# Kernel optimization log

Measured on AMD Instinct MI355X. Metric: run time of the kernel, lower is better.

Reference implementation:

```python
import jax, jax.numpy as jnp
import numpy as np

FS, R, ULAW = 160, 2, 256  # frame_size, n_samples_per_step, 2**ulaw


def _conv1d(x, w, b):
    # x: [B,C,L], w: [O,I,3], VALID conv (PyTorch Conv1d, no padding)
    y = jax.lax.conv_general_dilated(x, w, (1,), 'VALID',
                                     dimension_numbers=('NCH', 'OIH', 'NCH'))
    return y + b[None, :, None]


def _gru(x, Wih, Whh, bih, bhh):
    # PyTorch GRU (batch_first), gate order r,z,n. x: [B,T,In] -> [B,T,H]
    B = x.shape[0]
    H = Whh.shape[1]
    xW = jnp.einsum('bti,gi->btg', x, Wih) + bih  # precompute input gates [B,T,3H]
    def step(h, xw):
        gh = h @ Whh.T + bhh
        r = jax.nn.sigmoid(xw[:, :H] + gh[:, :H])
        z = jax.nn.sigmoid(xw[:, H:2 * H] + gh[:, H:2 * H])
        n = jnp.tanh(xw[:, 2 * H:] + r * gh[:, 2 * H:])
        h = (1.0 - z) * n + z * h
        return h, h
    h0 = jnp.zeros((B, H), x.dtype)
    _, ys = jax.lax.scan(step, h0, jnp.swapaxes(xW, 0, 1))
    return jnp.swapaxes(ys, 0, 1)


def _mdense(x, w1, w2, b1, b2, f1, f2):
    return jnp.tanh(x @ w1.T + b1) * f1 + jnp.tanh(x @ w2.T + b2) * f2


def setup_inputs() -> dict:
    key = jax.random.key(0)
    ks = jax.random.split(key, 40)
    B, NF, NBF = 64, 15, 20
    T = (NF - 4) * FS  # 1760: two VALID k=3 convs -> 11 frames
    EP, ES, DF, H1, H2 = 64, 128, 128, 384, 16
    IN_A = 3 * ES * R + DF   # 896
    IN_B = H1 + DF           # 512
    p = lambda k, shape, s=0.1: (s * jax.random.normal(k, shape)).astype(jnp.float32)
    d = {
        'in_data': jax.random.randint(ks[0], (B, T, 3), 0, ULAW),
        'features': jax.random.normal(ks[1], (B, NF, NBF), jnp.float32),
        'periods': jax.random.randint(ks[2], (B, NF, 1), 0, 256),
        'targets': jax.random.randint(ks[3], (B, T), 0, ULAW),
        'embed_pitch': p(ks[4], (256, EP)),
        'embed_sig': p(ks[5], (ULAW, ES)),
        'conv1_w': p(ks[6], (DF, EP + NBF, 3)), 'conv1_b': p(ks[7], (DF,)),
        'conv2_w': p(ks[8], (DF, DF, 3)), 'conv2_b': p(ks[9], (DF,)),
        'fd1_w': p(ks[10], (DF, DF)), 'fd1_b': p(ks[11], (DF,)),
        'fd2_w': p(ks[12], (DF, DF)), 'fd2_b': p(ks[13], (DF,)),
        'ga_wih': p(ks[14], (3 * H1, IN_A)), 'ga_whh': p(ks[15], (3 * H1, H1)),
        'ga_bih': p(ks[16], (3 * H1,)), 'ga_bhh': p(ks[17], (3 * H1,)),
        'gb_wih': p(ks[18], (3 * H2, IN_B)), 'gb_whh': p(ks[19], (3 * H2, H2)),
        'gb_bih': p(ks[20], (3 * H2,)), 'gb_bhh': p(ks[21], (3 * H2,)),
        'md1_w1': p(ks[22], (ULAW, H2)), 'md1_w2': p(ks[23], (ULAW, H2)),
        'md1_b1': p(ks[24], (ULAW,)), 'md1_b2': p(ks[25], (ULAW,)),
        'md1_f1': jnp.ones((ULAW,), jnp.float32), 'md1_f2': jnp.ones((ULAW,), jnp.float32),
        'md2_w1': p(ks[26], (ULAW, H2 + ES)), 'md2_w2': p(ks[27], (ULAW, H2 + ES)),
        'md2_b1': p(ks[28], (ULAW,)), 'md2_b2': p(ks[29], (ULAW,)),
        'md2_f1': jnp.ones((ULAW,), jnp.float32), 'md2_f2': jnp.ones((ULAW,), jnp.float32),
    }
    return d


def reference(in_data, features, periods, targets, embed_pitch, embed_sig,
              conv1_w, conv1_b, conv2_w, conv2_b, fd1_w, fd1_b, fd2_w, fd2_b,
              ga_wih, ga_whh, ga_bih, ga_bhh, gb_wih, gb_whh, gb_bih, gb_bhh,
              md1_w1, md1_w2, md1_b1, md1_b2, md1_f1, md1_f2,
              md2_w1, md2_w2, md2_b1, md2_b2, md2_f1, md2_f2):
    B, T = targets.shape
    # frame-rate feature network
    pitch = embed_pitch[periods[..., 0]]                  # [B,15,EP]
    cat = jnp.concatenate([features, pitch], axis=-1)      # [B,15,NBF+EP]
    x = jnp.swapaxes(cat, 1, 2)                            # [B,C,15]
    x = jnp.tanh(_conv1d(x, conv1_w, conv1_b))
    x = jnp.tanh(_conv1d(x, conv2_w, conv2_b))             # [B,DF,11]
    f = jnp.swapaxes(x, 1, 2)
    f = jnp.tanh(f @ fd1_w.T + fd1_b)
    f = jnp.tanh(f @ fd2_w.T + fd2_b)                      # [B,11,DF]
    rep = jnp.repeat(f, FS // R, axis=1)                   # [B,880,DF]
    # sample-rate network (bunched: R samples per step)
    emb = embed_sig[in_data].reshape(B, T, -1).reshape(B, T // R, -1)  # [B,880,3*ES*R]
    rnn_in = jnp.concatenate([emb, rep], axis=-1)
    g1 = _gru(rnn_in, ga_wih, ga_whh, ga_bih, ga_bhh)      # [B,880,H1]
    g2 = _gru(jnp.concatenate([g1, rep], axis=-1), gb_wih, gb_whh, gb_bih, gb_bhh)  # [B,880,H2]
    o1 = _mdense(g2, md1_w1, md1_w2, md1_b1, md1_b2, md1_f1, md1_f2)  # [B,880,ULAW]
    # teacher forcing (p_teacher_forcing = 1.0): even-index targets feed branch 2
    pred_exc = targets[:, 0::R]                            # [B,880]
    ctx = jnp.concatenate([g2, embed_sig[pred_exc]], axis=-1)
    o2 = _mdense(ctx, md2_w1, md2_w2, md2_b1, md2_b2, md2_f1, md2_f2)
    # strided scatter: out[:, ::2]=o1, out[:, 1::2]=o2 == interleave
    out = jnp.stack([o1, o2], axis=2).reshape(B, T, ULAW)
    return out
```

## Files before the change

### kernel.cpp

```cpp
#include <hip/hip_runtime.h>
#include <hip/hip_bf16.h>
#include <hip/hip_fp16.h>

#define NF    15
#define NBF   20
#define TT    1760
#define TS    880
#define EP    64
#define ES    128
#define DF    128
#define H1    384
#define G3    1152
#define INA   896
#define JREP  11

typedef _Float16 h2v __attribute__((ext_vector_type(2)));

__device__ __forceinline__ float sigmf_(float x){ return 1.0f/(1.0f + __expf(-x)); }
__device__ __forceinline__ float tanhf_(float x){ return 2.0f/(1.0f + __expf(-2.0f*x)) - 1.0f; }
__device__ __forceinline__ h2v bc_h2(unsigned u){ return __builtin_bit_cast(h2v, u); }
__device__ __forceinline__ float fdot2_(h2v a, h2v b, float c){
#if __has_builtin(__builtin_amdgcn_fdot2)
  return __builtin_amdgcn_fdot2(a, b, c, false);
#else
  return c + (float)a[0]*(float)b[0] + (float)a[1]*(float)b[1];
#endif
}
__device__ __forceinline__ unsigned pk2_(float a, float b){
#if __has_builtin(__builtin_amdgcn_cvt_pkrtz)
  return __builtin_bit_cast(unsigned, __builtin_amdgcn_cvt_pkrtz(a, b));
#else
  unsigned lo = (unsigned)__builtin_bit_cast(unsigned short, (_Float16)a);
  unsigned hi = (unsigned)__builtin_bit_cast(unsigned short, (_Float16)b);
  return lo | (hi << 16);
#endif
}
__device__ __forceinline__ void bar_lgkm(){
  asm volatile("s_waitcnt lgkmcnt(0)" ::: "memory");
  __builtin_amdgcn_s_barrier();
  __builtin_amdgcn_sched_barrier(0);
}

__global__ __launch_bounds__(128) void k_frame(const float* feat, const int* periods, const float* embp,
   const float* c1w, const float* c1b, const float* c2w, const float* c2b,
   const float* f1w, const float* f1b, const float* f2w, const float* f2b, float* fout)
{
  __shared__ float cat[NF*84];
  __shared__ float x1[13*DF];
  __shared__ float x2[JREP*DF];
  int b = blockIdx.x, tid = threadIdx.x;
  for (int idx = tid; idx < NF*84; idx += 128){
    int j = idx/84, c = idx%84;
    cat[idx] = (c < NBF) ? feat[(b*NF+j)*NBF + c]
                         : embp[periods[b*NF+j]*EP + (c-NBF)];
  }
  __syncthreads();
  int o = tid;
  for (int p = 0; p < 13; ++p){
    float acc = c1b[o];
    for (int kk = 0; kk < 3; ++kk)
      for (int c = 0; c < 84; ++c)
        acc += cat[(p+kk)*84 + c] * c1w[(o*84+c)*3+kk];
    x1[p*DF+o] = tanhf_(acc);
  }
  __syncthreads();
  for (int p = 0; p < JREP; ++p){
    float acc = c2b[o];
    for (int kk = 0; kk < 3; ++kk)
      for (int c = 0; c < DF; ++c)
        acc += x1[(p+kk)*DF+c] * c2w[(o*DF+c)*3+kk];
    x2[p*DF+o] = tanhf_(acc);
  }
  __syncthreads();
  for (int p = 0; p < JREP; ++p){
    float acc = f1b[o];
    for (int c = 0; c < DF; ++c) acc += x2[p*DF+c]*f1w[o*DF+c];
    x1[p*DF+o] = tanhf_(acc);
  }
  __syncthreads();
  for (int p = 0; p < JREP; ++p){
    float acc = f2b[o];
    for (int c = 0; c < DF; ++c) acc += x1[p*DF+c]*f2w[o*DF+c];
    fout[(b*JREP+p)*DF+o] = tanhf_(acc);
  }
}

__global__ __launch_bounds__(256) void k_wpack5(const float* whh, _Float16* wpk){
  int o = blockIdx.x*256 + threadIdx.x;
  int hu = o & 1;
  int c  = (o >> 1) & 3;
  int idx = o >> 3;
  int tid = idx % 768;
  int n   = (idx / 768) % 18;
  int hf  = idx / (768*18);
  int i = tid % 384, u = tid / 384;
  int gd = n*4 + c;
  int m = gd / 12, dc = gd % 12;
  int pos  = (dc % 2) + 2*(dc / 6);
  int gate = (dc % 6) >> 1;
  int j = hf*96 + u*48 + (4*m + pos)*2 + hu;
  wpk[o] = (_Float16)whh[(gate*H1 + i)*H1 + j];
}

__global__ __launch_bounds__(256) void k_tables(const float* wih, const float* emb, float* GA){
  __shared__ float Wl[64*129];
  int k = blockIdx.x/18, g0 = (blockIdx.x%18)*64;
  int tid = threadIdx.x;
  for (int idx = tid; idx < 64*128; idx += 256){
    int gg = idx>>7, c = idx&127;
    Wl[gg*129+c] = wih[(size_t)(g0+gg)*INA + k*128 + c];
  }
  __syncthreads();
  int vv = tid>>6, gg = tid&63;
  for (int v = vv; v < 256; v += 4){
    const float* e = emb + (size_t)v*ES;
    float acc = 0.f;
    for (int c = 0; c < 128; ++c) acc += e[c]*Wl[gg*129+c];
    GA[(size_t)(k*256+v)*G3 + g0+gg] = acc;
  }
}

__global__ __launch_bounds__(256) void k_xwrepA(const float* wih, const float* f,
                                                const float* bih, const float* bhh, float* xwA){
  __shared__ float Wl[64*129];
  int g0 = blockIdx.x*64, tid = threadIdx.x;
  for (int idx = tid; idx < 64*128; idx += 256){
    int gg = idx>>7, c = idx&127;
    Wl[gg*129+c] = wih[(size_t)(g0+gg)*INA + 768 + c];
  }
  __syncthreads();
  int vv = tid>>6, gg = tid&63; int g = g0+gg;
  float badd = bih[g] + (g < 768 ? bhh[g] : 0.f);
  for (int row = vv; row < 64*JREP; row += 4){
    const float* fr = f + (size_t)row*DF;
    float acc = badd;
    for (int c = 0; c < 128; ++c) acc += fr[c]*Wl[gg*129+c];
    xwA[(size_t)row*G3 + g] = acc;
  }
}

__global__ __launch_bounds__(256) void k_xwrepB(const float* wih, const float* f,
                                                const float* bih, const float* bhh, float* xwB){
  __shared__ float Wl[48*129];
  int b = blockIdx.x, tid = threadIdx.x;
  for (int idx = tid; idx < 48*128; idx += 256){
    int r = idx>>7, c = idx&127;
    Wl[r*129+c] = wih[r*512 + 384 + c];
  }
  __syncthreads();
  for (int idx = tid; idx < JREP*48; idx += 256){
    int j = idx/48, r = idx%48;
    const float* fr = f + (size_t)(b*JREP+j)*DF;
    float acc = bih[r] + (r < 32 ? bhh[r] : 0.f);
    for (int c = 0; c < 128; ++c) acc += fr[c]*Wl[r*129+c];
    xwB[(size_t)(b*JREP+j)*48 + r] = acc;
  }
}

__global__ __launch_bounds__(256) void k_t2(const float* w1, const float* w2, const float* emb, float* T2){
  __shared__ float Wl[64*129];
  int tbl = blockIdx.x>>2; int c0 = (blockIdx.x&3)*64; int tid = threadIdx.x;
  const float* w = tbl ? w2 : w1;
  for (int idx = tid; idx < 64*128; idx += 256){
    int cc = idx>>7, e = idx&127;
    Wl[cc*129+e] = w[(c0+cc)*144 + 16 + e];
  }
  __syncthreads();
  int vv = tid>>6, cc = tid&63;
  for (int v = vv; v < 256; v += 4){
    const float* e = emb + (size_t)v*ES;
    float acc = 0.f;
    for (int c = 0; c < 128; ++c) acc += e[c]*Wl[cc*129+c];
    T2[tbl*65536 + v*256 + c0+cc] = acc;
  }
}

#define LD18(n) uint4 d##n = wsrc[(size_t)(n)*768];
#define Q2(A,B,C, q2) { \
  h2v hA = hh[jb2 + (q2)*2],     hB = hh[jb2 + (q2)*2 + 1]; \
  ar = fdot2_(hA, bc_h2(A.x), ar); ar = fdot2_(hB, bc_h2(A.y), ar); \
  az = fdot2_(hA, bc_h2(A.z), az); az = fdot2_(hB, bc_h2(A.w), az); \
  an = fdot2_(hA, bc_h2(B.x), an); an = fdot2_(hB, bc_h2(B.y), an); \
  h2v hC = hh[jb2 + (q2)*2 + 2], hD = hh[jb2 + (q2)*2 + 3]; \
  ar = fdot2_(hC, bc_h2(B.z), ar); ar = fdot2_(hD, bc_h2(B.w), ar); \
  az = fdot2_(hC, bc_h2(C.x), az); az = fdot2_(hD, bc_h2(C.y), az); \
  an = fdot2_(hC, bc_h2(C.z), an); an = fdot2_(hD, bc_h2(C.w), an); }
#define DOTS12 \
  Q2(d0,d1,d2,0) Q2(d3,d4,d5,2) Q2(d6,d7,d8,4) \
  Q2(d9,d10,d11,6) Q2(d12,d13,d14,8) Q2(d15,d16,d17,10)

#define PLW(n, p) { unsigned w = __hip_atomic_load((p), __ATOMIC_RELAXED, __HIP_MEMORY_SCOPE_AGENT); \
                    rv##n = w; ok &= ((w & 1023u) == tg); }

__global__ __launch_bounds__(768, 3) void k_scanA9(const int* __restrict__ in_data,
        const float* __restrict__ GA, const float* __restrict__ xwA,
        const uint4* __restrict__ wpk, const float* __restrict__ bhh,
        unsigned* __restrict__ g1u, unsigned* pbuf)
{
  __shared__ __align__(16) unsigned h16u[48];
  __shared__ __align__(8)  float pg[3][2][384];
  __shared__ __align__(8)  float xwb[2][G3];
  __shared__ int indr[2][8];
  const int P = blockIdx.x;
  const int b = P & 63, hf = P >> 6;
  const int tid = threadIdx.x;
  const int i  = tid % 384;
  const int u  = tid / 384;
  const int jb2 = u * 24;
  const int* ind_b = in_data + (size_t)b*TT*3;

  const uint4* wsrc = wpk + (size_t)(hf*18)*768 + tid;
  LD18(0) LD18(1) LD18(2) LD18(3) LD18(4) LD18(5) LD18(6) LD18(7) LD18(8)
  LD18(9) LD18(10) LD18(11) LD18(12) LD18(13) LD18(14) LD18(15) LD18(16) LD18(17)

  const bool isGat = (tid < 576);
  const int  c0 = 2*tid, c1 = 2*tid + 1;
  const bool isPub = (tid >= 96 && tid < 672);
  const int  po0 = 2*(tid - 96);

  float hreg0 = 0.f, hreg1 = 0.f, bn0 = 0.f, bn1 = 0.f;
  if (tid < 48){
    bn0 = bhh[768 + hf*96 + 2*tid];
    bn1 = bhh[768 + hf*96 + 2*tid + 1];
    h16u[tid] = 0u;
  }
  if (isGat){
    float s0 = xwA[(size_t)(b*JREP)*G3 + c0];
    float s1 = xwA[(size_t)(b*JREP)*G3 + c1];
    #pragma unroll
    for (int k2 = 0; k2 < 6; ++k2){
      int v = ind_b[k2];
      s0 += GA[((size_t)k2*256 + v)*G3 + c0];
      s1 += GA[((size_t)k2*256 + v)*G3 + c1];
    }
    xwb[0][c0] = s0; xwb[0][c1] = s1;
  }
  if (tid >= 576 && tid < 582) indr[1][tid-576] = ind_b[6 + (tid-576)];

  unsigned* pbo = pbuf + ((size_t)(b*4 + hf)*2)*G3;
  const int pf1 = (hf+1)&3, pf2 = (hf+2)&3, pf3 = (hf+3)&3;
  const unsigned* pb1 = pbuf + ((size_t)(b*4 + pf1)*2)*G3 + hf*96 + 2*(tid<48?tid:0);
  const unsigned* pb2 = pbuf + ((size_t)(b*4 + pf2)*2)*G3 + hf*96 + 2*(tid<48?tid:0);
  const unsigned* pb3 = pbuf + ((size_t)(b*4 + pf3)*2)*G3 + hf*96 + 2*(tid<48?tid:0);
  const h2v* hh = (const h2v*)h16u;
  __syncthreads();

  for (int t = 0; t < TS; ++t){
    const int nb = t & 1;
    const int tp = t + 1;
    float ga0=0.f,ga1=0.f,ga2=0.f,ga3=0.f,ga4=0.f,ga5=0.f,gx0=0.f;
    float gb0=0.f,gb1=0.f,gb2=0.f,gb3=0.f,gb4=0.f,gb5=0.f,gx1=0.f;
    if (tp < TS && isGat){
      int v0=indr[tp&1][0], v1=indr[tp&1][1], v2=indr[tp&1][2];
      int v3=indr[tp&1][3], v4=indr[tp&1][4], v5=indr[tp&1][5];
      const float* xwr = xwA + ((size_t)(b*JREP) + tp/80)*G3;
      ga0 = GA[((size_t)0*256 + v0)*G3 + c0]; gb0 = GA[((size_t)0*256 + v0)*G3 + c1];
      ga1 = GA[((size_t)1*256 + v1)*G3 + c0]; gb1 = GA[((size_t)1*256 + v1)*G3 + c1];
      ga2 = GA[((size_t)2*256 + v2)*G3 + c0]; gb2 = GA[((size_t)2*256 + v2)*G3 + c1];
      ga3 = GA[((size_t)3*256 + v3)*G3 + c0]; gb3 = GA[((size_t)3*256 + v3)*G3 + c1];
      ga4 = GA[((size_t)4*256 + v4)*G3 + c0]; gb4 = GA[((size_t)4*256 + v4)*G3 + c1];
      ga5 = GA[((size_t)5*256 + v5)*G3 + c0]; gb5 = GA[((size_t)5*256 + v5)*G3 + c1];
      gx0 = xwr[c0]; gx1 = xwr[c1];
    }
    int iv = 0;
    const int stg = t + 2;
    const bool doStg = (tid >= 576 && tid < 582 && stg < TS);
    if (doStg) iv = ind_b[6*stg + (tid-576)];
    float ar=0.f, az=0.f, an=0.f;
    DOTS12
    pg[0][u][i] = ar; pg[1][u][i] = az; pg[2][u][i] = an;
    if (tp < TS && isGat){
      xwb[tp&1][c0] = ga0+ga1+ga2+ga3+ga4+ga5+gx0;
      xwb[tp&1][c1] = gb0+gb1+gb2+gb3+gb4+gb5+gx1;
    }
    if (doStg) indr[t&1][tid-576] = iv;
    bar_lgkm();
    if (isPub){
      int g = po0/384, ii = po0 - g*384;
      float2 p0 = *(const float2*)&pg[g][0][ii];
      float2 p1 = *(const float2*)&pg[g][1][ii];
      float v0 = p0.x + p1.x, v1 = p0.y + p1.y;
      unsigned tw0 = (__builtin_bit_cast(unsigned, v0) & 0xFFFFFC00u) | (unsigned)t;
      unsigned tw1 = (__builtin_bit_cast(unsigned, v1) & 0xFFFFFC00u) | (unsigned)t;
      unsigned* dst = pbo + (size_t)nb*G3 + po0;
      __hip_atomic_store(dst,     tw0, __ATOMIC_RELAXED, __HIP_MEMORY_SCOPE_AGENT);
      __hip_atomic_store(dst + 1, tw1, __ATOMIC_RELAXED, __HIP_MEMORY_SCOPE_AGENT);
    } else if (tid < 48){
      const unsigned tg = (unsigned)t;
      const unsigned* q1 = pb1 + (size_t)nb*G3;
      const unsigned* q2 = pb2 + (size_t)nb*G3;
      const unsigned* q3 = pb3 + (size_t)nb*G3;
      unsigned rv0,rv1,rv2,rv3,rv4,rv5,rv6,rv7,rv8;
      unsigned rv9,rv10,rv11,rv12,rv13,rv14,rv15,rv16,rv17;
      bool ok;
      do {
        ok = true;
        PLW(0,  q1+0) PLW(1,  q1+1) PLW(2,  q1+384) PLW(3,  q1+385) PLW(4,  q1+768) PLW(5,  q1+769)
        PLW(6,  q2+0) PLW(7,  q2+1) PLW(8,  q2+384) PLW(9,  q2+385) PLW(10, q2+768) PLW(11, q2+769)
        PLW(12, q3+0) PLW(13, q3+1) PLW(14, q3+384) PLW(15, q3+385) PLW(16, q3+768) PLW(17, q3+769)
        if (!ok) __builtin_amdgcn_s_sleep(1);
      } while (!ok);
      __builtin_amdgcn_sched_barrier(0);
      #define FV(n) __builtin_bit_cast(float, rv##n & 0xFFFFFC00u)
      int i0 = hf*96 + 2*tid;
      float2 o0 = *(const float2*)&pg[0][0][i0];  float2 o0b = *(const float2*)&pg[0][1][i0];
      float2 o1 = *(const float2*)&pg[1][0][i0];  float2 o1b = *(const float2*)&pg[1][1][i0];
      float2 o2 = *(const float2*)&pg[2][0][i0];  float2 o2b = *(const float2*)&pg[2][1][i0];
      float2 xr = *(const float2*)&xwb[nb][i0];
      float2 xz = *(const float2*)&xwb[nb][384 + i0];
      float2 xn = *(const float2*)&xwb[nb][768 + i0];
      float R0 = o0.x + o0b.x + FV(0)  + FV(6)  + FV(12) + xr.x;
      float R1 = o0.y + o0b.y + FV(1)  + FV(7)  + FV(13) + xr.y;
      float Z0 = o1.x + o1b.x + FV(2)  + FV(8)  + FV(14) + xz.x;
      float Z1 = o1.y + o1b.y + FV(3)  + FV(9)  + FV(15) + xz.y;
      float G0 = o2.x + o2b.x + FV(4)  + FV(10) + FV(16) + bn0;
      float G1 = o2.y + o2b.y + FV(5)  + FV(11) + FV(17) + bn1;
      #undef FV
      float rr0 = sigmf_(R0), zz0 = sigmf_(Z0);
      float nn0 = tanhf_(xn.x + rr0*G0);
      float h0 = (1.f - zz0)*nn0 + zz0*hreg0; hreg0 = h0;
      float rr1 = sigmf_(R1), zz1 = sigmf_(Z1);
      float nn1 = tanhf_(xn.y + rr1*G1);
      float h1 = (1.f - zz1)*nn1 + zz1*hreg1; hreg1 = h1;
      unsigned pack = pk2_(h0, h1);
      h16u[tid] = pack;
      g1u[((size_t)b*TS + t)*192 + hf*48 + tid] = pack;
    }
    bar_lgkm();
  }
}

__global__ __launch_bounds__(256) void k_xwB(const _Float16* g1, const float* wih,
                                             const float* xwrB, float* xwB){
  __shared__ _Float16 gl[16*392];
  int bi = blockIdx.x; int b = bi/55; int t0 = (bi%55)*16; int tid = threadIdx.x;
  for (int idx = tid; idx < 16*H1; idx += 256){
    int tt = idx/H1, c = idx%H1;
    gl[tt*392+c] = g1[((size_t)b*TS + t0+tt)*H1 + c];
  }
  __syncthreads();
  int rr = tid>>4, tt = tid&15;
  int t = t0+tt;
  const float* xr = xwrB + ((size_t)(b*JREP) + t/80)*48;
  for (int rb = 0; rb < 3; ++rb){
    int r = rb*16 + rr;
    const float* wrow = wih + (size_t)r*512;
    float acc = 0.f;
    for (int c = 0; c < H1; ++c) acc += (float)gl[tt*392+c]*wrow[c];
    xwB[((size_t)b*TS + t)*48 + r] = acc + xr[r];
  }
}

__global__ __launch_bounds__(64) void k_scanB(const float* xwB, const float* whh,
                                              const float* bhh, float* g2){
  __shared__ float wl[48*17];
  __shared__ float h2s[16];
  __shared__ float pre[32];
  __shared__ float xn[16], gn[16];
  int b = blockIdx.x, tid = threadIdx.x;
  for (int idx = tid; idx < 768; idx += 64) wl[(idx>>4)*17 + (idx&15)] = whh[idx];
  if (tid < 16) h2s[tid] = 0.f;
  float bn = (tid >= 32 && tid < 48) ? bhh[tid] : 0.f;
  __syncthreads();
  for (int t = 0; t < TS; ++t){
    if (tid < 48){
      float xw = xwB[((size_t)b*TS + t)*48 + tid];
      float gh = 0.f;
      for (int e = 0; e < 16; ++e) gh += wl[tid*17+e]*h2s[e];
      if (tid < 32) pre[tid] = xw + gh;
      else { xn[tid-32] = xw; gn[tid-32] = gh + bn; }
    }
    __syncthreads();
    if (tid < 16){
      float r = sigmf_(pre[tid]), z = sigmf_(pre[16+tid]);
      float n = tanhf_(xn[tid] + r*gn[tid]);
      float hn = (1.f - z)*n + z*h2s[tid];
      h2s[tid] = hn;
      g2[((size_t)b*TS + t)*16 + tid] = hn;
    }
    __syncthreads();
  }
}

__global__ __launch_bounds__(256) void k_out(const float* g2, const int* targets, const float* T2,
    const float* m1w1, const float* m1w2, const float* m1b1, const float* m1b2,
    const float* m1f1, const float* m1f2,
    const float* m2w1, const float* m2w2, const float* m2b1, const float* m2b2,
    const float* m2f1, const float* m2f2, float* out)
{
  __shared__ float wA[256*17], wB[256*17], wC[256*17], wD[256*17];
  __shared__ float g2l[16*16];
  int bi = blockIdx.x; int b = bi/55; int t0 = (bi%55)*16; int c = threadIdx.x;
  for (int d = 0; d < 16; ++d){
    wA[c*17+d] = m1w1[c*16+d];  wB[c*17+d] = m1w2[c*16+d];
    wC[c*17+d] = m2w1[c*144+d]; wD[c*17+d] = m2w2[c*144+d];
  }
  { int tt = c>>4, d = c&15; g2l[c] = g2[((size_t)b*TS + t0+tt)*16 + d]; }
  __syncthreads();
  float b1a = m1b1[c], b2a = m1b2[c], f1a = m1f1[c], f2a = m1f2[c];
  float b1b = m2b1[c], b2b = m2b2[c], f1b = m2f1[c], f2b = m2f2[c];
  for (int tt = 0; tt < 16; ++tt){
    int t = t0+tt;
    float d1 = b1a, d2 = b2a, e1 = b1b, e2 = b2b;
    for (int d = 0; d < 16; ++d){
      float g = g2l[tt*16+d];
      d1 += g*wA[c*17+d]; d2 += g*wB[c*17+d];
      e1 += g*wC[c*17+d]; e2 += g*wD[c*17+d];
    }
    int v = targets[b*TT + 2*t];
    e1 += T2[v*256+c]; e2 += T2[65536 + v*256+c];
    float o1 = f1a*tanhf_(d1) + f2a*tanhf_(d2);
    float o2 = f1b*tanhf_(e1) + f2b*tanhf_(e2);
    size_t base = ((size_t)b*TS + t)*2*256;
    out[base + c]       = o1;
    out[base + 256 + c] = o2;
  }
}

extern "C" void kernel_launch(void* const* d_in, const int* in_sizes, int n_in,
                              void* d_out, int out_size, void* d_ws, size_t ws_size,
                              hipStream_t stream) {
  const int*   in_data = (const int*)  d_in[0];
  const float* feat    = (const float*)d_in[1];
  const int*   periods = (const int*)  d_in[2];
  const int*   targets = (const int*)  d_in[3];
  const float* embp    = (const float*)d_in[4];
  const float* embs    = (const float*)d_in[5];
  const float* c1w = (const float*)d_in[6];  const float* c1b = (const float*)d_in[7];
  const float* c2w = (const float*)d_in[8];  const float* c2b = (const float*)d_in[9];
  const float* f1w = (const float*)d_in[10]; const float* f1b = (const float*)d_in[11];
  const float* f2w = (const float*)d_in[12]; const float* f2b = (const float*)d_in[13];
  const float* ga_wih = (const float*)d_in[14]; const float* ga_whh = (const float*)d_in[15];
  const float* ga_bih = (const float*)d_in[16]; const float* ga_bhh = (const float*)d_in[17];
  const float* gb_wih = (const float*)d_in[18]; const float* gb_whh = (const float*)d_in[19];
  const float* gb_bih = (const float*)d_in[20]; const float* gb_bhh = (const float*)d_in[21];
  const float* m1w1 = (const float*)d_in[22]; const float* m1w2 = (const float*)d_in[23];
  const float* m1b1 = (const float*)d_in[24]; const float* m1b2 = (const float*)d_in[25];
  const float* m1f1 = (const float*)d_in[26]; const float* m1f2 = (const float*)d_in[27];
  const float* m2w1 = (const float*)d_in[28]; const float* m2w2 = (const float*)d_in[29];
  const float* m2b1 = (const float*)d_in[30]; const float* m2b2 = (const float*)d_in[31];
  const float* m2f1 = (const float*)d_in[32]; const float* m2f2 = (const float*)d_in[33];
  float* out = (float*)d_out;

  float* GA     = (float*)d_ws;
  float* xWrepA = GA     + 1769472;
  float* xWrepB = xWrepA + 811008;
  float* fbuf   = xWrepB + 33792;
  float* xWB    = fbuf   + 90112;
  float* g2buf  = xWB    + 2703360;
  float* T2     = g2buf  + 901120;
  _Float16* Wpk = (_Float16*)(T2 + 131072);
  unsigned* pbuf = (unsigned*)(Wpk + 442368);
  _Float16* g1  = (_Float16*)d_out;

  (void)hipMemsetAsync(pbuf, 0xFF, 589824*sizeof(unsigned), stream);
  hipLaunchKernelGGL(k_frame, dim3(64), dim3(128), 0, stream,
                     feat, periods, embp, c1w, c1b, c2w, c2b, f1w, f1b, f2w, f2b, fbuf);
  hipLaunchKernelGGL(k_wpack5, dim3(1728), dim3(256), 0, stream, ga_whh, Wpk);
  hipLaunchKernelGGL(k_tables, dim3(108), dim3(256), 0, stream, ga_wih, embs, GA);
  hipLaunchKernelGGL(k_t2, dim3(8), dim3(256), 0, stream, m2w1, m2w2, embs, T2);
  hipLaunchKernelGGL(k_xwrepA, dim3(18), dim3(256), 0, stream, ga_wih, fbuf, ga_bih, ga_bhh, xWrepA);
  hipLaunchKernelGGL(k_xwrepB, dim3(64), dim3(256), 0, stream, gb_wih, fbuf, gb_bih, gb_bhh, xWrepB);
  hipLaunchKernelGGL(k_scanA9, dim3(256), dim3(768), 0, stream,
                     in_data, GA, xWrepA, (const uint4*)Wpk, ga_bhh,
                     (unsigned*)g1, pbuf);
  hipLaunchKernelGGL(k_xwB, dim3(64*55), dim3(256), 0, stream, g1, gb_wih, xWrepB, xWB);
  hipLaunchKernelGGL(k_scanB, dim3(64), dim3(64), 0, stream, xWB, gb_whh, gb_bhh, g2buf);
  hipLaunchKernelGGL(k_out, dim3(64*55), dim3(256), 0, stream,
                     g2buf, targets, T2, m1w1, m1w2, m1b1, m1b2, m1f1, m1f2,
                     m2w1, m2w2, m2b1, m2b2, m2f1, m2f2, out);
}
```

Measured before the change: 4.094 ms.

## Widen scan flag polls, pack xwB weights to fp16 dot2, shuffle-based scanB

The scanA poll loop now reads each pair of adjacent tagged words with one 64-bit atomic load instead of two 32-bit loads, and the step tag is masked to 10 bits. k_xwB stages the GRU-B input weights into shared memory as packed fp16 pairs and uses fdot2 instead of scalar fp32 loads from global memory. k_scanB keeps its recurrent weights in registers and exchanges state with wave shuffles instead of shared memory and two __syncthreads per step, and it prefetches the next xw value. Together these target polling latency, global weight traffic and per-step barrier cost, at the price of fp16 rounding of the B-layer input weights.

```diff
diff --git a/kernel.cpp b/kernel.cpp
--- a/kernel.cpp
+++ b/kernel.cpp
@@ -15,6 +15,7 @@
 #define JREP  11
 
 typedef _Float16 h2v __attribute__((ext_vector_type(2)));
+typedef unsigned long long u64;
 
 __device__ __forceinline__ float sigmf_(float x){ return 1.0f/(1.0f + __expf(-x)); }
 __device__ __forceinline__ float tanhf_(float x){ return 2.0f/(1.0f + __expf(-2.0f*x)) - 1.0f; }
@@ -189,10 +190,11 @@
   Q2(d0,d1,d2,0) Q2(d3,d4,d5,2) Q2(d6,d7,d8,4) \
   Q2(d9,d10,d11,6) Q2(d12,d13,d14,8) Q2(d15,d16,d17,10)
 
-#define PLW(n, p) { unsigned w = __hip_atomic_load((p), __ATOMIC_RELAXED, __HIP_MEMORY_SCOPE_AGENT); \
-                    rv##n = w; ok &= ((w & 1023u) == tg); }
-
-__global__ __launch_bounds__(768, 3) void k_scanA9(const int* __restrict__ in_data,
+#define PL2(na, nb_, p) { u64 w2 = __hip_atomic_load((const u64*)(p), __ATOMIC_RELAXED, __HIP_MEMORY_SCOPE_AGENT); \
+  rv##na = (unsigned)w2; rv##nb_ = (unsigned)(w2 >> 32); \
+  ok &= ((rv##na & 1023u) == tg) & ((rv##nb_ & 1023u) == tg); }
+
+__global__ __launch_bounds__(768, 3) void k_scanA13(const int* __restrict__ in_data,
         const float* __restrict__ GA, const float* __restrict__ xwA,
         const uint4* __restrict__ wpk, const float* __restrict__ bhh,
         unsigned* __restrict__ g1u, unsigned* pbuf)
@@ -280,13 +282,13 @@
       float2 p0 = *(const float2*)&pg[g][0][ii];
       float2 p1 = *(const float2*)&pg[g][1][ii];
       float v0 = p0.x + p1.x, v1 = p0.y + p1.y;
-      unsigned tw0 = (__builtin_bit_cast(unsigned, v0) & 0xFFFFFC00u) | (unsigned)t;
-      unsigned tw1 = (__builtin_bit_cast(unsigned, v1) & 0xFFFFFC00u) | (unsigned)t;
+      unsigned tw0 = (__builtin_bit_cast(unsigned, v0) & 0xFFFFFC00u) | (unsigned)(t & 1023);
+      unsigned tw1 = (__builtin_bit_cast(unsigned, v1) & 0xFFFFFC00u) | (unsigned)(t & 1023);
       unsigned* dst = pbo + (size_t)nb*G3 + po0;
       __hip_atomic_store(dst,     tw0, __ATOMIC_RELAXED, __HIP_MEMORY_SCOPE_AGENT);
       __hip_atomic_store(dst + 1, tw1, __ATOMIC_RELAXED, __HIP_MEMORY_SCOPE_AGENT);
     } else if (tid < 48){
-      const unsigned tg = (unsigned)t;
+      const unsigned tg = (unsigned)t & 1023u;
       const unsigned* q1 = pb1 + (size_t)nb*G3;
       const unsigned* q2 = pb2 + (size_t)nb*G3;
       const unsigned* q3 = pb3 + (size_t)nb*G3;
@@ -295,9 +297,9 @@
       bool ok;
       do {
         ok = true;
-        PLW(0,  q1+0) PLW(1,  q1+1) PLW(2,  q1+384) PLW(3,  q1+385) PLW(4,  q1+768) PLW(5,  q1+769)
-        PLW(6,  q2+0) PLW(7,  q2+1) PLW(8,  q2+384) PLW(9,  q2+385) PLW(10, q2+768) PLW(11, q2+769)
-        PLW(12, q3+0) PLW(13, q3+1) PLW(14, q3+384) PLW(15, q3+385) PLW(16, q3+768) PLW(17, q3+769)
+        PL2(0,1,   q1+0) PL2(2,3,   q1+384) PL2(4,5,   q1+768)
+        PL2(6,7,   q2+0) PL2(8,9,   q2+384) PL2(10,11, q2+768)
+        PL2(12,13, q3+0) PL2(14,15, q3+384) PL2(16,17, q3+768)
         if (!ok) __builtin_amdgcn_s_sleep(1);
       } while (!ok);
       __builtin_amdgcn_sched_barrier(0);
@@ -330,55 +332,69 @@
   }
 }
 
-__global__ __launch_bounds__(256) void k_xwB(const _Float16* g1, const float* wih,
+__global__ __launch_bounds__(256) void k_xwB(const unsigned* g1u, const float* wih,
                                              const float* xwrB, float* xwB){
-  __shared__ _Float16 gl[16*392];
+  __shared__ __align__(16) unsigned gl[16*194];
+  __shared__ __align__(16) unsigned wl[48*194];
   int bi = blockIdx.x; int b = bi/55; int t0 = (bi%55)*16; int tid = threadIdx.x;
-  for (int idx = tid; idx < 16*H1; idx += 256){
-    int tt = idx/H1, c = idx%H1;
-    gl[tt*392+c] = g1[((size_t)b*TS + t0+tt)*H1 + c];
+  for (int idx = tid; idx < 48*192; idx += 256){
+    int r = idx/192, cp = idx%192;
+    wl[r*194+cp] = pk2_(wih[r*512 + 2*cp], wih[r*512 + 2*cp + 1]);
+  }
+  for (int idx = tid; idx < 16*192; idx += 256){
+    int tt = idx/192, c = idx%192;
+    gl[tt*194+c] = g1u[((size_t)b*TS + t0+tt)*192 + c];
   }
   __syncthreads();
   int rr = tid>>4, tt = tid&15;
   int t = t0+tt;
   const float* xr = xwrB + ((size_t)(b*JREP) + t/80)*48;
+  const h2v* gp = (const h2v*)&gl[tt*194];
   for (int rb = 0; rb < 3; ++rb){
     int r = rb*16 + rr;
-    const float* wrow = wih + (size_t)r*512;
+    const h2v* wp_ = (const h2v*)&wl[r*194];
     float acc = 0.f;
-    for (int c = 0; c < H1; ++c) acc += (float)gl[tt*392+c]*wrow[c];
+    #pragma unroll 8
+    for (int c = 0; c < 192; ++c) acc = fdot2_(gp[c], wp_[c], acc);
     xwB[((size_t)b*TS + t)*48 + r] = acc + xr[r];
   }
 }
 
 __global__ __launch_bounds__(64) void k_scanB(const float* xwB, const float* whh,
                                               const float* bhh, float* g2){
-  __shared__ float wl[48*17];
-  __shared__ float h2s[16];
-  __shared__ float pre[32];
-  __shared__ float xn[16], gn[16];
   int b = blockIdx.x, tid = threadIdx.x;
-  for (int idx = tid; idx < 768; idx += 64) wl[(idx>>4)*17 + (idx&15)] = whh[idx];
-  if (tid < 16) h2s[tid] = 0.f;
-  float bn = (tid >= 32 && tid < 48) ? bhh[tid] : 0.f;
-  __syncthreads();
+  float w0=0,w1=0,w2=0,w3=0,w4=0,w5=0,w6=0,w7=0;
+  float w8=0,w9=0,w10=0,w11=0,w12=0,w13=0,w14=0,w15=0;
+  if (tid < 48){
+    const float* wr = whh + tid*16;
+    w0=wr[0];w1=wr[1];w2=wr[2];w3=wr[3];w4=wr[4];w5=wr[5];w6=wr[6];w7=wr[7];
+    w8=wr[8];w9=wr[9];w10=wr[10];w11=wr[11];w12=wr[12];w13=wr[13];w14=wr[14];w15=wr[15];
+  }
+  float bng = (tid < 16) ? bhh[32 + tid] : 0.f;
+  float hv = 0.f;
+  float xw_n = (tid < 48) ? xwB[(size_t)b*TS*48 + tid] : 0.f;
   for (int t = 0; t < TS; ++t){
-    if (tid < 48){
-      float xw = xwB[((size_t)b*TS + t)*48 + tid];
-      float gh = 0.f;
-      for (int e = 0; e < 16; ++e) gh += wl[tid*17+e]*h2s[e];
-      if (tid < 32) pre[tid] = xw + gh;
-      else { xn[tid-32] = xw; gn[tid-32] = gh + bn; }
-    }
-    __syncthreads();
+    float xw = xw_n;
+    if (t+1 < TS && tid < 48) xw_n = xwB[((size_t)b*TS + t+1)*48 + tid];
+    float gh = 0.f;
+    gh += w0 *__shfl(hv, 0, 64);  gh += w1 *__shfl(hv, 1, 64);
+    gh += w2 *__shfl(hv, 2, 64);  gh += w3 *__shfl(hv, 3, 64);
+    gh += w4 *__shfl(hv, 4, 64);  gh += w5 *__shfl(hv, 5, 64);
+    gh += w6 *__shfl(hv, 6, 64);  gh += w7 *__shfl(hv, 7, 64);
+    gh += w8 *__shfl(hv, 8, 64);  gh += w9 *__shfl(hv, 9, 64);
+    gh += w10*__shfl(hv,10, 64);  gh += w11*__shfl(hv,11, 64);
+    gh += w12*__shfl(hv,12, 64);  gh += w13*__shfl(hv,13, 64);
+    gh += w14*__shfl(hv,14, 64);  gh += w15*__shfl(hv,15, 64);
+    float val = xw + gh;
+    float zv  = __shfl(val, (tid+16) & 63, 64);
+    float xn_ = __shfl(xw,  (tid+32) & 63, 64);
+    float gn_ = __shfl(gh,  (tid+32) & 63, 64) + bng;
     if (tid < 16){
-      float r = sigmf_(pre[tid]), z = sigmf_(pre[16+tid]);
-      float n = tanhf_(xn[tid] + r*gn[tid]);
-      float hn = (1.f - z)*n + z*h2s[tid];
-      h2s[tid] = hn;
-      g2[((size_t)b*TS + t)*16 + tid] = hn;
-    }
-    __syncthreads();
+      float r = sigmf_(val), z = sigmf_(zv);
+      float n = tanhf_(xn_ + r*gn_);
+      hv = (1.f - z)*n + z*hv;
+      g2[((size_t)b*TS + t)*16 + tid] = hv;
+    }
   }
 }
 
@@ -461,10 +477,11 @@
   hipLaunchKernelGGL(k_t2, dim3(8), dim3(256), 0, stream, m2w1, m2w2, embs, T2);
   hipLaunchKernelGGL(k_xwrepA, dim3(18), dim3(256), 0, stream, ga_wih, fbuf, ga_bih, ga_bhh, xWrepA);
   hipLaunchKernelGGL(k_xwrepB, dim3(64), dim3(256), 0, stream, gb_wih, fbuf, gb_bih, gb_bhh, xWrepB);
-  hipLaunchKernelGGL(k_scanA9, dim3(256), dim3(768), 0, stream,
+  hipLaunchKernelGGL(k_scanA13, dim3(256), dim3(768), 0, stream,
                      in_data, GA, xWrepA, (const uint4*)Wpk, ga_bhh,
                      (unsigned*)g1, pbuf);
-  hipLaunchKernelGGL(k_xwB, dim3(64*55), dim3(256), 0, stream, g1, gb_wih, xWrepB, xWB);
+  hipLaunchKernelGGL(k_xwB, dim3(64*55), dim3(256), 0, stream,
+                     (const unsigned*)g1, gb_wih, xWrepB, xWB);
   hipLaunchKernelGGL(k_scanB, dim3(64), dim3(64), 0, stream, xWB, gb_whh, gb_bhh, g2buf);
   hipLaunchKernelGGL(k_out, dim3(64*55), dim3(256), 0, stream,
                      g2buf, targets, T2, m1w1, m1w2, m1b1, m1b2, m1f1, m1f2,
```

Result: faster. 3.645 ms (-11.0%).
